# Optimization experiments

Hardware: AMD Instinct MI355X
Metric: run time of the kernel (lower is better)

Reference implementation:

```python
import jax, jax.numpy as jnp
import numpy as np

D = 1024
LD = 64
NTR = 8192
NT = 8192
DY = 128

def setup_inputs() -> dict:
    key = jax.random.key(0)
    k1, k2, k3, k4 = jax.random.split(key, 4)
    xtr = jax.random.normal(k1, (NTR, D), dtype=jnp.float32)
    ytr = jax.random.normal(k2, (NTR, DY), dtype=jnp.float32)
    xt = jax.random.normal(k3, (NT, D), dtype=jnp.float32)
    A = jax.random.normal(k4, (D, LD), dtype=jnp.float32) / (D ** 0.5)
    return {"xtr": xtr, "ytr": ytr, "xt": xt, "A": A}

def reference(xtr, ytr, xt, A):
    # mean-center both train and test features with the train mean
    mu = jnp.mean(xtr, axis=0, keepdims=True)          # [1, d]
    qtr = (xtr - mu) @ A                                # [Ntr, ld]
    qt = (xt - mu) @ A                                  # [Nt, ld]
    scores = jnp.einsum('nl,ml->nm', qt, qtr)           # [Nt, Ntr]
    E = jax.nn.softmax(scores, axis=1)                  # row-wise softmax over train points
    return E @ ytr                                      # [Nt, dy]
```

## Files before the change

kernel.cpp:

```cpp
#include <hip/hip_runtime.h>
#include <hip/hip_bf16.h>

#define D    1024
#define LD   64
#define NTR  8192
#define NT   8192
#define DY   128

#define SHIFT 40.0f

typedef __attribute__((ext_vector_type(8))) short bf16x8;
typedef __attribute__((ext_vector_type(8))) _Float16 half8;
typedef __attribute__((ext_vector_type(4))) short short4_;
typedef __attribute__((ext_vector_type(4))) float f4;

static __device__ __forceinline__ short f2bf(float f) {
    __hip_bfloat16 h = __float2bfloat16(f);
    short s; __builtin_memcpy(&s, &h, 2); return s;
}
static __device__ __forceinline__ float bf2f(short s) {
    __hip_bfloat16 h; __builtin_memcpy(&h, &s, 2); return __bfloat162float(h);
}
static __device__ __forceinline__ short f2h(float f) {
    _Float16 h = (_Float16)f;
    short s; __builtin_memcpy(&s, &h, 2); return s;
}
static __device__ __forceinline__ float h2f(short s) {
    _Float16 h; __builtin_memcpy(&h, &s, 2); return (float)h;
}

static __device__ __forceinline__ void gload_lds16(const void* g, void* l) {
    __builtin_amdgcn_global_load_lds(
        (const __attribute__((address_space(1))) unsigned int*)g,
        (__attribute__((address_space(3))) unsigned int*)l,
        16, 0, 0);
}

__global__ __launch_bounds__(256) void a_prep(const float* __restrict__ A,
                                              short* __restrict__ Afh,
                                              short* __restrict__ Afl) {
    int idx = blockIdx.x * 256 + threadIdx.x;
    float a = A[idx];
    int k = idx >> 6;
    int col = idx & 63;
    short hi = f2bf(a);
    short lo = f2bf(a - bf2f(hi));
    int o = ((k >> 6) * 8 + ((k >> 5) & 1) * 4 + ((k >> 3) & 3)) * 512
          + col * 8 + (k & 7);
    Afh[o] = hi;
    Afl[o] = lo;
}

__global__ __launch_bounds__(256) void proj_prep(const float* __restrict__ xt,
                                                 const float* __restrict__ xtr,
                                                 const short* __restrict__ Afh,
                                                 const short* __restrict__ Afl,
                                                 const float* __restrict__ ytr,
                                                 short* __restrict__ qt_hi,
                                                 short* __restrict__ qt_lo,
                                                 short* __restrict__ ktr,
                                                 float* __restrict__ muAp,
                                                 short* __restrict__ vtile) {
    __shared__ __align__(16) char smraw[32768];

    int tid = threadIdx.x;
    int b = blockIdx.x;

    if (b >= 512) {
        float* tile = (float*)smraw;
        int bz = b - 512;
        int t0 = (bz & 127) * 64;
        int d0 = (bz >> 7) * 64;
        int c = tid & 63;
        int r4 = tid >> 6;
        #pragma unroll
        for (int i = 0; i < 16; ++i) {
            int r = i * 4 + r4;
            tile[r * 66 + c] = ytr[(long)(t0 + r) * DY + d0 + c];
        }
        __syncthreads();
        #pragma unroll
        for (int i = 0; i < 16; ++i) {
            int r = i * 4 + r4;
            int t = t0 + c;
            int dy = d0 + r;
            long idx = (long)(t >> 5) * 4096 + (long)dy * 32
                     + ((((t >> 3) & 3) ^ (dy & 3)) << 3) + (t & 7);
            vtile[idx] = f2bf(tile[c * 66 + r]);
        }
        return;
    }

    short (*xh)[32][128] = (short (*)[32][128])smraw;
    short (*xl)[32][128] = (short (*)[32][128])(smraw + 16384);

    int wave = tid >> 6;
    int lane = tid & 63;
    int quad = lane >> 4;
    int l16 = lane & 15;

    bool is_test = b < 256;
    int row0 = (is_test ? b : b - 256) * 32;
    const float* x = is_test ? xt : xtr;

    int crow = tid >> 3;
    int cg0 = tid & 7;
    const float* xg = x + (long)(row0 + crow) * D + cg0 * 8;
    int sw0 = ((cg0)     ^ (crow & 7)) * 8;
    int sw1 = ((cg0 + 8) ^ (crow & 7)) * 8;

    int col = wave * 16 + l16;
    const short* AfhL = Afh + quad * 512 + col * 8;
    const short* AflL = Afl + quad * 512 + col * 8;

    f4 acc[2][2];
    #pragma unroll
    for (int rt = 0; rt < 2; ++rt)
        #pragma unroll
        for (int s2 = 0; s2 < 2; ++s2)
            acc[rt][s2] = (f4){0.f, 0.f, 0.f, 0.f};

    {
        f4 v0 = *(const f4*)xg;
        f4 v1 = *(const f4*)(xg + 4);
        f4 v2 = *(const f4*)(xg + 64);
        f4 v3 = *(const f4*)(xg + 68);
        bf16x8 h0, l0, h1, l1;
        #pragma unroll
        for (int e = 0; e < 4; ++e) {
            h0[e]     = f2bf(v0[e]);  l0[e]     = f2bf(v0[e] - bf2f(h0[e]));
            h0[e + 4] = f2bf(v1[e]);  l0[e + 4] = f2bf(v1[e] - bf2f(h0[e + 4]));
            h1[e]     = f2bf(v2[e]);  l1[e]     = f2bf(v2[e] - bf2f(h1[e]));
            h1[e + 4] = f2bf(v3[e]);  l1[e + 4] = f2bf(v3[e] - bf2f(h1[e + 4]));
        }
        *(bf16x8*)&xh[0][crow][sw0] = h0;
        *(bf16x8*)&xl[0][crow][sw0] = l0;
        *(bf16x8*)&xh[0][crow][sw1] = h1;
        *(bf16x8*)&xl[0][crow][sw1] = l1;
    }
    __syncthreads();

    #pragma unroll 1
    for (int s = 0; s < 8; ++s) {
        int cur = s & 1;

        f4 nv0, nv1, nv2, nv3;
        if (s < 7) {
            const float* ng = xg + (s + 1) * 128;
            nv0 = *(const f4*)ng;
            nv1 = *(const f4*)(ng + 4);
            nv2 = *(const f4*)(ng + 64);
            nv3 = *(const f4*)(ng + 68);
        }

        #pragma unroll
        for (int s2 = 0; s2 < 2; ++s2) {
            int s2g = s * 2 + s2;

            bf16x8 bh0 = *(const bf16x8*)(AfhL + s2g * 4096);
            bf16x8 bh1 = *(const bf16x8*)(AfhL + s2g * 4096 + 2048);
            bf16x8 bl0 = *(const bf16x8*)(AflL + s2g * 4096);
            bf16x8 bl1 = *(const bf16x8*)(AflL + s2g * 4096 + 2048);

            int ch0 = s2 * 8 + quad;
            int sx0 = ((ch0)     ^ (l16 & 7)) * 8;
            int sx1 = ((ch0 + 4) ^ (l16 & 7)) * 8;

            #pragma unroll
            for (int rt = 0; rt < 2; ++rt) {
                const short* xhr = &xh[cur][rt * 16 + l16][0];
                const short* xlr = &xl[cur][rt * 16 + l16][0];
                bf16x8 ah0 = *(const bf16x8*)(xhr + sx0);
                bf16x8 ah1 = *(const bf16x8*)(xhr + sx1);
                bf16x8 al0 = *(const bf16x8*)(xlr + sx0);
                bf16x8 al1 = *(const bf16x8*)(xlr + sx1);

                acc[rt][s2] = __builtin_amdgcn_mfma_f32_16x16x32_bf16(ah0, bh0, acc[rt][s2], 0, 0, 0);
                acc[rt][s2] = __builtin_amdgcn_mfma_f32_16x16x32_bf16(al0, bh0, acc[rt][s2], 0, 0, 0);
                acc[rt][s2] = __builtin_amdgcn_mfma_f32_16x16x32_bf16(ah0, bl0, acc[rt][s2], 0, 0, 0);
                acc[rt][s2] = __builtin_amdgcn_mfma_f32_16x16x32_bf16(ah1, bh1, acc[rt][s2], 0, 0, 0);
                acc[rt][s2] = __builtin_amdgcn_mfma_f32_16x16x32_bf16(al1, bh1, acc[rt][s2], 0, 0, 0);
                acc[rt][s2] = __builtin_amdgcn_mfma_f32_16x16x32_bf16(ah1, bl1, acc[rt][s2], 0, 0, 0);
            }
        }

        if (s < 7) {
            bf16x8 h0, l0, h1, l1;
            #pragma unroll
            for (int e = 0; e < 4; ++e) {
                h0[e]     = f2bf(nv0[e]);  l0[e]     = f2bf(nv0[e] - bf2f(h0[e]));
                h0[e + 4] = f2bf(nv1[e]);  l0[e + 4] = f2bf(nv1[e] - bf2f(h0[e + 4]));
                h1[e]     = f2bf(nv2[e]);  l1[e]     = f2bf(nv2[e] - bf2f(h1[e]));
                h1[e + 4] = f2bf(nv3[e]);  l1[e + 4] = f2bf(nv3[e] - bf2f(h1[e + 4]));
            }
            *(bf16x8*)&xh[cur ^ 1][crow][sw0] = h0;
            *(bf16x8*)&xl[cur ^ 1][crow][sw0] = l0;
            *(bf16x8*)&xh[cur ^ 1][crow][sw1] = h1;
            *(bf16x8*)&xl[cur ^ 1][crow][sw1] = l1;
        }
        __syncthreads();
    }

    #pragma unroll
    for (int rt = 0; rt < 2; ++rt) {
        f4 q4 = acc[rt][0] + acc[rt][1];
        #pragma unroll
        for (int r = 0; r < 4; ++r) {
            int grow = row0 + rt * 16 + quad * 4 + r;
            float qv = q4[r];
            if (is_test) {
                short hi = f2h(qv);
                qt_hi[(long)grow * LD + col] = hi;
                qt_lo[(long)grow * LD + col] = f2h(qv - h2f(hi));
            } else {
                int tl = grow & 31;
                long idx = (long)(grow >> 5) * 2048 + tl * 64
                         + ((((col >> 3) ^ (tl & 7))) << 3) + (col & 7);
                ktr[idx] = f2h(qv);
            }
        }
    }

    if (!is_test) {
        f4 t4 = (acc[0][0] + acc[0][1]) + (acc[1][0] + acc[1][1]);
        float s = t4[0] + t4[1] + t4[2] + t4[3];
        s += __shfl_xor(s, 16);
        s += __shfl_xor(s, 32);
        if (quad == 0) muAp[(long)(b - 256) * 64 + col] = s;
    }
}

__global__ __launch_bounds__(256) void c_kernel(const short* __restrict__ ktr,
                                                const float* __restrict__ muAp,
                                                float* __restrict__ cc) {
    __shared__ float red[4][64];
    __shared__ __align__(16) float muAs[64];
    int l = threadIdx.x & 63;
    int g = threadIdx.x >> 6;
    float ms = 0.f;
    #pragma unroll 8
    for (int p = g; p < 256; p += 4) ms += muAp[(long)p * 64 + l];
    red[g][l] = ms;
    __syncthreads();
    if (threadIdx.x < 64)
        muAs[l] = (red[0][l] + red[1][l] + red[2][l] + red[3][l]) *
                  (1.0f / (float)NTR);
    __syncthreads();

    int t = blockIdx.x * 256 + threadIdx.x;
    int tl = t & 31;
    long rb = (long)(t >> 5) * 2048 + tl * 64;
    float s = SHIFT;
    #pragma unroll
    for (int c = 0; c < 8; ++c) {
        int pos = (c ^ (tl & 7)) << 3;
        bf16x8 h8 = *(const bf16x8*)&ktr[rb + pos];
        f4 m0 = *(const f4*)&muAs[c * 8];
        f4 m1 = *(const f4*)&muAs[c * 8 + 4];
        #pragma unroll
        for (int j = 0; j < 4; ++j) {
            s += h2f(h8[j]) * m0[j];
            s += h2f(h8[j + 4]) * m1[j];
        }
    }
    cc[t] = s;
}

template<int NC>
__global__ __launch_bounds__(256, 3) void flash_kernel(const short* __restrict__ qt_hi,
                                                       const short* __restrict__ qt_lo,
                                                       const short* __restrict__ ksw,
                                                       const short* __restrict__ vtile,
                                                       const float* __restrict__ cc,
                                                       short* __restrict__ Opart,
                                                       float* __restrict__ Lpart) {
    constexpr int TPC = 256 / NC;
    constexpr int CH  = NTR / NC;

    __shared__ __align__(16) short kbh[2][2048];
    __shared__ __align__(16) short vbuf[2][4096];
    __shared__ __align__(16) short ptile[4][1280];

    int tid = threadIdx.x;
    int wave = tid >> 6;
    int lane = tid & 63;
    int quad = lane >> 4;
    int l16 = lane & 15;

    int kc = blockIdx.x & (NC - 1);
    int qi = blockIdx.x / NC;
    int q0w = qi * 128 + wave * 32;
    int tile0 = kc * TPC;
    int kc0 = kc * CH;

    int soff = wave * 512 + lane * 8;
    int ldso = wave * 512;

    half8 qh[2][2], ql[2][2];
    #pragma unroll
    for (int rt = 0; rt < 2; ++rt) {
        const short* qrh = qt_hi + (long)(q0w + rt * 16 + l16) * LD + quad * 8;
        const short* qrl = qt_lo + (long)(q0w + rt * 16 + l16) * LD + quad * 8;
        qh[rt][0] = *(const half8*)qrh;
        qh[rt][1] = *(const half8*)(qrh + 32);
        ql[rt][0] = *(const half8*)qrl;
        ql[rt][1] = *(const half8*)(qrl + 32);
    }

    bf16x8 onef;
    #pragma unroll
    for (int i = 0; i < 8; ++i) onef[i] = (short)0x3F80;

    f4 Ov[2][8];
    f4 Lv[2];
    #pragma unroll
    for (int rt = 0; rt < 2; ++rt) {
        Lv[rt] = (f4){0.f, 0.f, 0.f, 0.f};
        #pragma unroll
        for (int jt = 0; jt < 8; ++jt) Ov[rt][jt] = (f4){0.f, 0.f, 0.f, 0.f};
    }

    short* myp = &ptile[wave][0];
    const int p0 = ((quad ^ (l16 & 7)) << 3);
    const int pv = ((quad ^ (l16 & 3)) << 3);

    gload_lds16(ksw + (long)tile0 * 2048 + soff, &kbh[0][ldso]);
    gload_lds16(vtile + (long)tile0 * 4096 + soff, &vbuf[0][ldso]);
    gload_lds16(vtile + (long)tile0 * 4096 + 2048 + soff, &vbuf[0][2048 + ldso]);
    __syncthreads();

    #pragma unroll 1
    for (int it = 0; it < TPC; ++it) {
        int cur = it & 1;

        f4 cv[2];
        #pragma unroll
        for (int tt = 0; tt < 2; ++tt)
            cv[tt] = *(const f4*)&cc[kc0 + it * 32 + tt * 16 + quad * 4];

        if (it < TPC - 1) {
            int nb = cur ^ 1;
            long tb = (long)(tile0 + it + 1);
            gload_lds16(ksw + tb * 2048 + soff, &kbh[nb][ldso]);
            gload_lds16(vtile + tb * 4096 + soff, &vbuf[nb][ldso]);
            gload_lds16(vtile + tb * 4096 + 2048 + soff, &vbuf[nb][2048 + ldso]);
        }

        half8 kh[2][2];
        #pragma unroll
        for (int tt = 0; tt < 2; ++tt) {
            int rb = (tt * 16 + l16) * 64;
            kh[tt][0] = *(const half8*)&kbh[cur][rb + p0];
            kh[tt][1] = *(const half8*)&kbh[cur][rb + (p0 ^ 32)];
        }

        f4 s[2][2];
        #pragma unroll
        for (int rt = 0; rt < 2; ++rt) {
            #pragma unroll
            for (int tt = 0; tt < 2; ++tt) {
                f4 a = (f4){0.f, 0.f, 0.f, 0.f};
                a = __builtin_amdgcn_mfma_f32_16x16x32_f16(kh[tt][0], qh[rt][0], a, 0, 0, 0);
                a = __builtin_amdgcn_mfma_f32_16x16x32_f16(kh[tt][0], ql[rt][0], a, 0, 0, 0);
                a = __builtin_amdgcn_mfma_f32_16x16x32_f16(kh[tt][1], qh[rt][1], a, 0, 0, 0);
                a = __builtin_amdgcn_mfma_f32_16x16x32_f16(kh[tt][1], ql[rt][1], a, 0, 0, 0);
                s[rt][tt] = a;
            }
        }

        #pragma unroll
        for (int rt = 0; rt < 2; ++rt) {
            #pragma unroll
            for (int tt = 0; tt < 2; ++tt) {
                short4_ p4;
                p4[0] = f2bf(__expf(s[rt][tt][0] - cv[tt][0]));
                p4[1] = f2bf(__expf(s[rt][tt][1] - cv[tt][1]));
                p4[2] = f2bf(__expf(s[rt][tt][2] - cv[tt][2]));
                p4[3] = f2bf(__expf(s[rt][tt][3] - cv[tt][3]));
                *(short4_*)&myp[(rt * 16 + l16) * 40 + tt * 16 + quad * 4] = p4;
            }
        }

        bf16x8 vf[8];
        #pragma unroll
        for (int jt = 0; jt < 8; ++jt)
            vf[jt] = *(const bf16x8*)&vbuf[cur][(jt * 16 + l16) * 32 + pv];
        #pragma unroll
        for (int rt = 0; rt < 2; ++rt) {
            bf16x8 pf = *(const bf16x8*)&myp[(rt * 16 + l16) * 40 + quad * 8];
            #pragma unroll
            for (int jt = 0; jt < 8; ++jt)
                Ov[rt][jt] = __builtin_amdgcn_mfma_f32_16x16x32_bf16(pf, vf[jt], Ov[rt][jt], 0, 0, 0);
            Lv[rt] = __builtin_amdgcn_mfma_f32_16x16x32_bf16(pf, onef, Lv[rt], 0, 0, 0);
        }

        __syncthreads();
    }

    long ob = (long)kc * NT;
    #pragma unroll
    for (int rt = 0; rt < 2; ++rt) {
        #pragma unroll
        for (int jt = 0; jt < 8; ++jt) {
            #pragma unroll
            for (int r = 0; r < 4; ++r)
                Opart[(ob + q0w + rt * 16 + quad * 4 + r) * DY + jt * 16 + l16] =
                    f2bf(Ov[rt][jt][r]);
        }
        if (l16 == 0) {
            #pragma unroll
            for (int r = 0; r < 4; ++r)
                Lpart[ob + q0w + rt * 16 + quad * 4 + r] = Lv[rt][r];
        }
    }
}

template<int NC>
__global__ __launch_bounds__(256) void finalize_kernel(const short* __restrict__ Opart,
                                                       const float* __restrict__ Lpart,
                                                       float* __restrict__ out) {
    long i = ((long)blockIdx.x * 256 + threadIdx.x) * 8;
    long row = i >> 7;
    float L = 0.f;
    f4 a = (f4){0.f, 0.f, 0.f, 0.f};
    f4 b = (f4){0.f, 0.f, 0.f, 0.f};
    #pragma unroll
    for (int kc = 0; kc < NC; ++kc) {
        L += Lpart[(long)kc * NT + row];
        bf16x8 o = *(const bf16x8*)&Opart[(long)kc * NT * DY + i];
        #pragma unroll
        for (int j = 0; j < 4; ++j) {
            a[j] += bf2f(o[j]);
            b[j] += bf2f(o[j + 4]);
        }
    }
    float linv = 1.0f / L;
    a *= linv; b *= linv;
    *(f4*)&out[i] = a;
    *(f4*)&out[i + 4] = b;
}

extern "C" void kernel_launch(void* const* d_in, const int* in_sizes, int n_in,
                              void* d_out, int out_size, void* d_ws, size_t ws_size,
                              hipStream_t stream) {
    const float* xtr = (const float*)d_in[0];
    const float* ytr = (const float*)d_in[1];
    const float* xt  = (const float*)d_in[2];
    const float* A   = (const float*)d_in[3];
    float* out = (float*)d_out;

    const size_t need16 =
        (size_t)512 * 64 * 4 + (size_t)NTR * 4 +
        (size_t)16 * NT * 4 + (size_t)16 * NT * DY * 2 +
        (size_t)NT * LD * 2 * 2 + (size_t)NTR * LD * 2 +
        (size_t)DY * NTR * 2 + (size_t)D * LD * 2 * 2;
    const int NC = (ws_size >= need16) ? 16 : 8;

    char* w = (char*)d_ws;
    float* muAp  = (float*)w; w += (size_t)512 * 64 * 4;
    float* cc    = (float*)w; w += (size_t)NTR * 4;
    float* Lpart = (float*)w; w += (size_t)NC * NT * 4;
    short* Opart = (short*)w; w += (size_t)NC * NT * DY * 2;
    short* qt_hi  = (short*)w; w += (size_t)NT * LD * 2;
    short* qt_lo  = (short*)w; w += (size_t)NT * LD * 2;
    short* ksw    = (short*)w; w += (size_t)NTR * LD * 2;
    short* vtile  = (short*)w; w += (size_t)DY * NTR * 2;
    short* Afh    = (short*)w; w += (size_t)D * LD * 2;
    short* Afl    = (short*)w; w += (size_t)D * LD * 2;
    (void)in_sizes; (void)n_in; (void)out_size;

    a_prep<<<256, 256, 0, stream>>>(A, Afh, Afl);
    proj_prep<<<768, 256, 0, stream>>>(xt, xtr, Afh, Afl, ytr,
                                       qt_hi, qt_lo, ksw, muAp, vtile);
    c_kernel<<<32, 256, 0, stream>>>(ksw, muAp, cc);
    if (NC == 16) {
        flash_kernel<16><<<64 * 16, 256, 0, stream>>>(qt_hi, qt_lo, ksw, vtile,
                                                      cc, Opart, Lpart);
        finalize_kernel<16><<<(NT * DY) / (256 * 8), 256, 0, stream>>>(Opart,
                                                                       Lpart, out);
    } else {
        flash_kernel<8><<<64 * 8, 256, 0, stream>>>(qt_hi, qt_lo, ksw, vtile,
                                                    cc, Opart, Lpart);
        finalize_kernel<8><<<(NT * DY) / (256 * 8), 256, 0, stream>>>(Opart,
                                                                      Lpart, out);
    }
}
```

Before: 161.6 us.

## Merge prep and flash/finalize stages into cooperative kernels with grid sync

Replaces the five separate launches with two cooperative kernels: one runs A prep, projection and the c-shift computation separated by grid-wide syncs, the other runs the flash attention pass with NC=8 followed by a grid sync and the finalize reduction. The aim is to cut kernel launch gaps and tail idle time between stages. The flash path now always uses 8 key chunks, giving 512 blocks instead of 1024, which lowers parallelism. It also relies on every block being co-resident for the grid sync, and falls back to separate launches if the cooperative launch fails.

```diff
diff --git a/kernel.cpp b/kernel.cpp
--- a/kernel.cpp
+++ b/kernel.cpp
@@ -1,5 +1,8 @@
 #include <hip/hip_runtime.h>
 #include <hip/hip_bf16.h>
+#include <hip/hip_cooperative_groups.h>
+
+namespace cg = cooperative_groups;
 
 #define D    1024
 #define LD   64
@@ -36,10 +39,11 @@
         16, 0, 0);
 }
 
-__global__ __launch_bounds__(256) void a_prep(const float* __restrict__ A,
-                                              short* __restrict__ Afh,
-                                              short* __restrict__ Afl) {
-    int idx = blockIdx.x * 256 + threadIdx.x;
+
+static __device__ __forceinline__ void aprep_body(const float* __restrict__ A,
+                                                  short* __restrict__ Afh,
+                                                  short* __restrict__ Afl,
+                                                  int idx) {
     float a = A[idx];
     int k = idx >> 6;
     int col = idx & 63;
@@ -51,20 +55,18 @@
     Afl[o] = lo;
 }
 
-__global__ __launch_bounds__(256) void proj_prep(const float* __restrict__ xt,
-                                                 const float* __restrict__ xtr,
-                                                 const short* __restrict__ Afh,
-                                                 const short* __restrict__ Afl,
-                                                 const float* __restrict__ ytr,
-                                                 short* __restrict__ qt_hi,
-                                                 short* __restrict__ qt_lo,
-                                                 short* __restrict__ ktr,
-                                                 float* __restrict__ muAp,
-                                                 short* __restrict__ vtile) {
+static __device__ void proj_body(const float* __restrict__ xt,
+                                 const float* __restrict__ xtr,
+                                 const short* __restrict__ Afh,
+                                 const short* __restrict__ Afl,
+                                 const float* __restrict__ ytr,
+                                 short* __restrict__ qt_hi,
+                                 short* __restrict__ qt_lo,
+                                 short* __restrict__ ktr,
+                                 float* __restrict__ muAp,
+                                 short* __restrict__ vtile,
+                                 int b, int tid) {
     __shared__ __align__(16) char smraw[32768];
-
-    int tid = threadIdx.x;
-    int b = blockIdx.x;
 
     if (b >= 512) {
         float* tile = (float*)smraw;
@@ -230,24 +232,24 @@
     }
 }
 
-__global__ __launch_bounds__(256) void c_kernel(const short* __restrict__ ktr,
-                                                const float* __restrict__ muAp,
-                                                float* __restrict__ cc) {
+static __device__ void c_body(const short* __restrict__ ktr,
+                              const float* __restrict__ muAp,
+                              float* __restrict__ cc, int bid, int tid) {
     __shared__ float red[4][64];
     __shared__ __align__(16) float muAs[64];
-    int l = threadIdx.x & 63;
-    int g = threadIdx.x >> 6;
+    int l = tid & 63;
+    int g = tid >> 6;
     float ms = 0.f;
     #pragma unroll 8
     for (int p = g; p < 256; p += 4) ms += muAp[(long)p * 64 + l];
     red[g][l] = ms;
     __syncthreads();
-    if (threadIdx.x < 64)
+    if (tid < 64)
         muAs[l] = (red[0][l] + red[1][l] + red[2][l] + red[3][l]) *
                   (1.0f / (float)NTR);
     __syncthreads();
 
-    int t = blockIdx.x * 256 + threadIdx.x;
+    int t = bid * 256 + tid;
     int tl = t & 31;
     long rb = (long)(t >> 5) * 2048 + tl * 64;
     float s = SHIFT;
@@ -264,6 +266,242 @@
         }
     }
     cc[t] = s;
+}
+
+template<int NC>
+static __device__ void flash_body(const short* __restrict__ qt_hi,
+                                  const short* __restrict__ qt_lo,
+                                  const short* __restrict__ ksw,
+                                  const short* __restrict__ vtile,
+                                  const float* __restrict__ cc,
+                                  short* __restrict__ Opart,
+                                  float* __restrict__ Lpart,
+                                  int bid, int tid) {
+    constexpr int TPC = 256 / NC;
+    constexpr int CH  = NTR / NC;
+
+    __shared__ __align__(16) short kbh[2][2048];
+    __shared__ __align__(16) short vbuf[2][4096];
+    __shared__ __align__(16) short ptile[4][1280];
+
+    int wave = tid >> 6;
+    int lane = tid & 63;
+    int quad = lane >> 4;
+    int l16 = lane & 15;
+
+    int kc = bid & (NC - 1);
+    int qi = bid / NC;
+    int q0w = qi * 128 + wave * 32;
+    int tile0 = kc * TPC;
+    int kc0 = kc * CH;
+
+    int soff = wave * 512 + lane * 8;
+    int ldso = wave * 512;
+
+    half8 qh[2][2], ql[2][2];
+    #pragma unroll
+    for (int rt = 0; rt < 2; ++rt) {
+        const short* qrh = qt_hi + (long)(q0w + rt * 16 + l16) * LD + quad * 8;
+        const short* qrl = qt_lo + (long)(q0w + rt * 16 + l16) * LD + quad * 8;
+        qh[rt][0] = *(const half8*)qrh;
+        qh[rt][1] = *(const half8*)(qrh + 32);
+        ql[rt][0] = *(const half8*)qrl;
+        ql[rt][1] = *(const half8*)(qrl + 32);
+    }
+
+    bf16x8 onef;
+    #pragma unroll
+    for (int i = 0; i < 8; ++i) onef[i] = (short)0x3F80;
+
+    f4 Ov[2][8];
+    f4 Lv[2];
+    #pragma unroll
+    for (int rt = 0; rt < 2; ++rt) {
+        Lv[rt] = (f4){0.f, 0.f, 0.f, 0.f};
+        #pragma unroll
+        for (int jt = 0; jt < 8; ++jt) Ov[rt][jt] = (f4){0.f, 0.f, 0.f, 0.f};
+    }
+
+    short* myp = &ptile[wave][0];
+    const int p0 = ((quad ^ (l16 & 7)) << 3);
+    const int pv = ((quad ^ (l16 & 3)) << 3);
+
+    gload_lds16(ksw + (long)tile0 * 2048 + soff, &kbh[0][ldso]);
+    gload_lds16(vtile + (long)tile0 * 4096 + soff, &vbuf[0][ldso]);
+    gload_lds16(vtile + (long)tile0 * 4096 + 2048 + soff, &vbuf[0][2048 + ldso]);
+    __syncthreads();
+
+    #pragma unroll 1
+    for (int it = 0; it < TPC; ++it) {
+        int cur = it & 1;
+
+        f4 cv[2];
+        #pragma unroll
+        for (int tt = 0; tt < 2; ++tt)
+            cv[tt] = *(const f4*)&cc[kc0 + it * 32 + tt * 16 + quad * 4];
+
+        if (it < TPC - 1) {
+            int nb = cur ^ 1;
+            long tb = (long)(tile0 + it + 1);
+            gload_lds16(ksw + tb * 2048 + soff, &kbh[nb][ldso]);
+            gload_lds16(vtile + tb * 4096 + soff, &vbuf[nb][ldso]);
+            gload_lds16(vtile + tb * 4096 + 2048 + soff, &vbuf[nb][2048 + ldso]);
+        }
+
+        half8 kh[2][2];
+        #pragma unroll
+        for (int tt = 0; tt < 2; ++tt) {
+            int rb = (tt * 16 + l16) * 64;
+            kh[tt][0] = *(const half8*)&kbh[cur][rb + p0];
+            kh[tt][1] = *(const half8*)&kbh[cur][rb + (p0 ^ 32)];
+        }
+
+        f4 s[2][2];
+        #pragma unroll
+        for (int rt = 0; rt < 2; ++rt) {
+            #pragma unroll
+            for (int tt = 0; tt < 2; ++tt) {
+                f4 a = (f4){0.f, 0.f, 0.f, 0.f};
+                a = __builtin_amdgcn_mfma_f32_16x16x32_f16(kh[tt][0], qh[rt][0], a, 0, 0, 0);
+                a = __builtin_amdgcn_mfma_f32_16x16x32_f16(kh[tt][0], ql[rt][0], a, 0, 0, 0);
+                a = __builtin_amdgcn_mfma_f32_16x16x32_f16(kh[tt][1], qh[rt][1], a, 0, 0, 0);
+                a = __builtin_amdgcn_mfma_f32_16x16x32_f16(kh[tt][1], ql[rt][1], a, 0, 0, 0);
+                s[rt][tt] = a;
+            }
+        }
+
+        #pragma unroll
+        for (int rt = 0; rt < 2; ++rt) {
+            #pragma unroll
+            for (int tt = 0; tt < 2; ++tt) {
+                short4_ p4;
+                p4[0] = f2bf(__expf(s[rt][tt][0] - cv[tt][0]));
+                p4[1] = f2bf(__expf(s[rt][tt][1] - cv[tt][1]));
+                p4[2] = f2bf(__expf(s[rt][tt][2] - cv[tt][2]));
+                p4[3] = f2bf(__expf(s[rt][tt][3] - cv[tt][3]));
+                *(short4_*)&myp[(rt * 16 + l16) * 40 + tt * 16 + quad * 4] = p4;
+            }
+        }
+
+        bf16x8 vf[8];
+        #pragma unroll
+        for (int jt = 0; jt < 8; ++jt)
+            vf[jt] = *(const bf16x8*)&vbuf[cur][(jt * 16 + l16) * 32 + pv];
+        #pragma unroll
+        for (int rt = 0; rt < 2; ++rt) {
+            bf16x8 pf = *(const bf16x8*)&myp[(rt * 16 + l16) * 40 + quad * 8];
+            #pragma unroll
+            for (int jt = 0; jt < 8; ++jt)
+                Ov[rt][jt] = __builtin_amdgcn_mfma_f32_16x16x32_bf16(pf, vf[jt], Ov[rt][jt], 0, 0, 0);
+            Lv[rt] = __builtin_amdgcn_mfma_f32_16x16x32_bf16(pf, onef, Lv[rt], 0, 0, 0);
+        }
+
+        __syncthreads();
+    }
+
+    long ob = (long)kc * NT;
+    #pragma unroll
+    for (int rt = 0; rt < 2; ++rt) {
+        #pragma unroll
+        for (int jt = 0; jt < 8; ++jt) {
+            #pragma unroll
+            for (int r = 0; r < 4; ++r)
+                Opart[(ob + q0w + rt * 16 + quad * 4 + r) * DY + jt * 16 + l16] =
+                    f2bf(Ov[rt][jt][r]);
+        }
+        if (l16 == 0) {
+            #pragma unroll
+            for (int r = 0; r < 4; ++r)
+                Lpart[ob + q0w + rt * 16 + quad * 4 + r] = Lv[rt][r];
+        }
+    }
+}
+
+template<int NC>
+static __device__ void finalize_body(const short* __restrict__ Opart,
+                                     const float* __restrict__ Lpart,
+                                     float* __restrict__ out, int bid, int tid) {
+    long i = ((long)bid * 256 + tid) * 8;
+    long row = i >> 7;
+    float L = 0.f;
+    f4 a = (f4){0.f, 0.f, 0.f, 0.f};
+    f4 b = (f4){0.f, 0.f, 0.f, 0.f};
+    #pragma unroll
+    for (int kc = 0; kc < NC; ++kc) {
+        L += Lpart[(long)kc * NT + row];
+        bf16x8 o = *(const bf16x8*)&Opart[(long)kc * NT * DY + i];
+        #pragma unroll
+        for (int j = 0; j < 4; ++j) {
+            a[j] += bf2f(o[j]);
+            b[j] += bf2f(o[j + 4]);
+        }
+    }
+    float linv = 1.0f / L;
+    a *= linv; b *= linv;
+    *(f4*)&out[i] = a;
+    *(f4*)&out[i + 4] = b;
+}
+
+
+__global__ __launch_bounds__(256, 3) void prep_all(const float* __restrict__ xt,
+                                                   const float* __restrict__ xtr,
+                                                   const float* __restrict__ A,
+                                                   const float* __restrict__ ytr,
+                                                   short* __restrict__ qt_hi,
+                                                   short* __restrict__ qt_lo,
+                                                   short* __restrict__ ktr,
+                                                   float* __restrict__ muAp,
+                                                   short* __restrict__ vtile,
+                                                   short* __restrict__ Afh,
+                                                   short* __restrict__ Afl,
+                                                   float* __restrict__ cc) {
+    int gi = blockIdx.x * 256 + threadIdx.x;
+    if (gi < 65536) aprep_body(A, Afh, Afl, gi);
+    cg::this_grid().sync();
+    proj_body(xt, xtr, Afh, Afl, ytr, qt_hi, qt_lo, ktr, muAp, vtile,
+              blockIdx.x, threadIdx.x);
+    cg::this_grid().sync();
+    if (blockIdx.x < 32) c_body(ktr, muAp, cc, blockIdx.x, threadIdx.x);
+}
+
+__global__ __launch_bounds__(256, 3) void flash_fin(const short* __restrict__ qt_hi,
+                                                    const short* __restrict__ qt_lo,
+                                                    const short* __restrict__ ksw,
+                                                    const short* __restrict__ vtile,
+                                                    const float* __restrict__ cc,
+                                                    short* __restrict__ Opart,
+                                                    float* __restrict__ Lpart,
+                                                    float* __restrict__ out) {
+    flash_body<8>(qt_hi, qt_lo, ksw, vtile, cc, Opart, Lpart,
+                  blockIdx.x, threadIdx.x);
+    cg::this_grid().sync();
+    finalize_body<8>(Opart, Lpart, out, blockIdx.x, threadIdx.x);
+}
+
+__global__ __launch_bounds__(256) void a_prep(const float* __restrict__ A,
+                                              short* __restrict__ Afh,
+                                              short* __restrict__ Afl) {
+    aprep_body(A, Afh, Afl, blockIdx.x * 256 + threadIdx.x);
+}
+
+__global__ __launch_bounds__(256) void proj_prep(const float* __restrict__ xt,
+                                                 const float* __restrict__ xtr,
+                                                 const short* __restrict__ Afh,
+                                                 const short* __restrict__ Afl,
+                                                 const float* __restrict__ ytr,
+                                                 short* __restrict__ qt_hi,
+                                                 short* __restrict__ qt_lo,
+                                                 short* __restrict__ ktr,
+                                                 float* __restrict__ muAp,
+                                                 short* __restrict__ vtile) {
+    proj_body(xt, xtr, Afh, Afl, ytr, qt_hi, qt_lo, ktr, muAp, vtile,
+              blockIdx.x, threadIdx.x);
+}
+
+__global__ __launch_bounds__(256) void c_kernel(const short* __restrict__ ktr,
+                                                const float* __restrict__ muAp,
+                                                float* __restrict__ cc) {
+    c_body(ktr, muAp, cc, blockIdx.x, threadIdx.x);
 }
 
 template<int NC>
@@ -274,170 +512,15 @@
                                                        const float* __restrict__ cc,
                                                        short* __restrict__ Opart,
                                                        float* __restrict__ Lpart) {
-    constexpr int TPC = 256 / NC;
-    constexpr int CH  = NTR / NC;
-
-    __shared__ __align__(16) short kbh[2][2048];
-    __shared__ __align__(16) short vbuf[2][4096];
-    __shared__ __align__(16) short ptile[4][1280];
-
-    int tid = threadIdx.x;
-    int wave = tid >> 6;
-    int lane = tid & 63;
-    int quad = lane >> 4;
-    int l16 = lane & 15;
-
-    int kc = blockIdx.x & (NC - 1);
-    int qi = blockIdx.x / NC;
-    int q0w = qi * 128 + wave * 32;
-    int tile0 = kc * TPC;
-    int kc0 = kc * CH;
-
-    int soff = wave * 512 + lane * 8;
-    int ldso = wave * 512;
-
-    half8 qh[2][2], ql[2][2];
-    #pragma unroll
-    for (int rt = 0; rt < 2; ++rt) {
-        const short* qrh = qt_hi + (long)(q0w + rt * 16 + l16) * LD + quad * 8;
-        const short* qrl = qt_lo + (long)(q0w + rt * 16 + l16) * LD + quad * 8;
-        qh[rt][0] = *(const half8*)qrh;
-        qh[rt][1] = *(const half8*)(qrh + 32);
-        ql[rt][0] = *(const half8*)qrl;
-        ql[rt][1] = *(const half8*)(qrl + 32);
-    }
-
-    bf16x8 onef;
-    #pragma unroll
-    for (int i = 0; i < 8; ++i) onef[i] = (short)0x3F80;
-
-    f4 Ov[2][8];
-    f4 Lv[2];
-    #pragma unroll
-    for (int rt = 0; rt < 2; ++rt) {
-        Lv[rt] = (f4){0.f, 0.f, 0.f, 0.f};
-        #pragma unroll
-        for (int jt = 0; jt < 8; ++jt) Ov[rt][jt] = (f4){0.f, 0.f, 0.f, 0.f};
-    }
-
-    short* myp = &ptile[wave][0];
-    const int p0 = ((quad ^ (l16 & 7)) << 3);
-    const int pv = ((quad ^ (l16 & 3)) << 3);
-
-    gload_lds16(ksw + (long)tile0 * 2048 + soff, &kbh[0][ldso]);
-    gload_lds16(vtile + (long)tile0 * 4096 + soff, &vbuf[0][ldso]);
-    gload_lds16(vtile + (long)tile0 * 4096 + 2048 + soff, &vbuf[0][2048 + ldso]);
-    __syncthreads();
-
-    #pragma unroll 1
-    for (int it = 0; it < TPC; ++it) {
-        int cur = it & 1;
-
-        f4 cv[2];
-        #pragma unroll
-        for (int tt = 0; tt < 2; ++tt)
-            cv[tt] = *(const f4*)&cc[kc0 + it * 32 + tt * 16 + quad * 4];
-
-        if (it < TPC - 1) {
-            int nb = cur ^ 1;
-            long tb = (long)(tile0 + it + 1);
-            gload_lds16(ksw + tb * 2048 + soff, &kbh[nb][ldso]);
-            gload_lds16(vtile + tb * 4096 + soff, &vbuf[nb][ldso]);
-            gload_lds16(vtile + tb * 4096 + 2048 + soff, &vbuf[nb][2048 + ldso]);
-        }
-
-        half8 kh[2][2];
-        #pragma unroll
-        for (int tt = 0; tt < 2; ++tt) {
-            int rb = (tt * 16 + l16) * 64;
-            kh[tt][0] = *(const half8*)&kbh[cur][rb + p0];
-            kh[tt][1] = *(const half8*)&kbh[cur][rb + (p0 ^ 32)];
-        }
-
-        f4 s[2][2];
-        #pragma unroll
-        for (int rt = 0; rt < 2; ++rt) {
-            #pragma unroll
-            for (int tt = 0; tt < 2; ++tt) {
-                f4 a = (f4){0.f, 0.f, 0.f, 0.f};
-                a = __builtin_amdgcn_mfma_f32_16x16x32_f16(kh[tt][0], qh[rt][0], a, 0, 0, 0);
-                a = __builtin_amdgcn_mfma_f32_16x16x32_f16(kh[tt][0], ql[rt][0], a, 0, 0, 0);
-                a = __builtin_amdgcn_mfma_f32_16x16x32_f16(kh[tt][1], qh[rt][1], a, 0, 0, 0);
-                a = __builtin_amdgcn_mfma_f32_16x16x32_f16(kh[tt][1], ql[rt][1], a, 0, 0, 0);
-                s[rt][tt] = a;
-            }
-        }
-
-        #pragma unroll
-        for (int rt = 0; rt < 2; ++rt) {
-            #pragma unroll
-            for (int tt = 0; tt < 2; ++tt) {
-                short4_ p4;
-                p4[0] = f2bf(__expf(s[rt][tt][0] - cv[tt][0]));
-                p4[1] = f2bf(__expf(s[rt][tt][1] - cv[tt][1]));
-                p4[2] = f2bf(__expf(s[rt][tt][2] - cv[tt][2]));
-                p4[3] = f2bf(__expf(s[rt][tt][3] - cv[tt][3]));
-                *(short4_*)&myp[(rt * 16 + l16) * 40 + tt * 16 + quad * 4] = p4;
-            }
-        }
-
-        bf16x8 vf[8];
-        #pragma unroll
-        for (int jt = 0; jt < 8; ++jt)
-            vf[jt] = *(const bf16x8*)&vbuf[cur][(jt * 16 + l16) * 32 + pv];
-        #pragma unroll
-        for (int rt = 0; rt < 2; ++rt) {
-            bf16x8 pf = *(const bf16x8*)&myp[(rt * 16 + l16) * 40 + quad * 8];
-            #pragma unroll
-            for (int jt = 0; jt < 8; ++jt)
-                Ov[rt][jt] = __builtin_amdgcn_mfma_f32_16x16x32_bf16(pf, vf[jt], Ov[rt][jt], 0, 0, 0);
-            Lv[rt] = __builtin_amdgcn_mfma_f32_16x16x32_bf16(pf, onef, Lv[rt], 0, 0, 0);
-        }
-
-        __syncthreads();
-    }
-
-    long ob = (long)kc * NT;
-    #pragma unroll
-    for (int rt = 0; rt < 2; ++rt) {
-        #pragma unroll
-        for (int jt = 0; jt < 8; ++jt) {
-            #pragma unroll
-            for (int r = 0; r < 4; ++r)
-                Opart[(ob + q0w + rt * 16 + quad * 4 + r) * DY + jt * 16 + l16] =
-                    f2bf(Ov[rt][jt][r]);
-        }
-        if (l16 == 0) {
-            #pragma unroll
-            for (int r = 0; r < 4; ++r)
-                Lpart[ob + q0w + rt * 16 + quad * 4 + r] = Lv[rt][r];
-        }
-    }
+    flash_body<NC>(qt_hi, qt_lo, ksw, vtile, cc, Opart, Lpart,
+                   blockIdx.x, threadIdx.x);
 }
 
 template<int NC>
 __global__ __launch_bounds__(256) void finalize_kernel(const short* __restrict__ Opart,
                                                        const float* __restrict__ Lpart,
                                                        float* __restrict__ out) {
-    long i = ((long)blockIdx.x * 256 + threadIdx.x) * 8;
-    long row = i >> 7;
-    float L = 0.f;
-    f4 a = (f4){0.f, 0.f, 0.f, 0.f};
-    f4 b = (f4){0.f, 0.f, 0.f, 0.f};
-    #pragma unroll
-    for (int kc = 0; kc < NC; ++kc) {
-        L += Lpart[(long)kc * NT + row];
-        bf16x8 o = *(const bf16x8*)&Opart[(long)kc * NT * DY + i];
-        #pragma unroll
-        for (int j = 0; j < 4; ++j) {
-            a[j] += bf2f(o[j]);
-            b[j] += bf2f(o[j + 4]);
-        }
-    }
-    float linv = 1.0f / L;
-    a *= linv; b *= linv;
-    *(f4*)&out[i] = a;
-    *(f4*)&out[i + 4] = b;
+    finalize_body<NC>(Opart, Lpart, out, blockIdx.x, threadIdx.x);
 }
 
 extern "C" void kernel_launch(void* const* d_in, const int* in_sizes, int n_in,
@@ -454,13 +537,13 @@
         (size_t)16 * NT * 4 + (size_t)16 * NT * DY * 2 +
         (size_t)NT * LD * 2 * 2 + (size_t)NTR * LD * 2 +
         (size_t)DY * NTR * 2 + (size_t)D * LD * 2 * 2;
-    const int NC = (ws_size >= need16) ? 16 : 8;
+    const int NCF = (ws_size >= need16) ? 16 : 8;
 
     char* w = (char*)d_ws;
     float* muAp  = (float*)w; w += (size_t)512 * 64 * 4;
     float* cc    = (float*)w; w += (size_t)NTR * 4;
-    float* Lpart = (float*)w; w += (size_t)NC * NT * 4;
-    short* Opart = (short*)w; w += (size_t)NC * NT * DY * 2;
+    float* Lpart = (float*)w; w += (size_t)NCF * NT * 4;
+    short* Opart = (short*)w; w += (size_t)NCF * NT * DY * 2;
     short* qt_hi  = (short*)w; w += (size_t)NT * LD * 2;
     short* qt_lo  = (short*)w; w += (size_t)NT * LD * 2;
     short* ksw    = (short*)w; w += (size_t)NTR * LD * 2;
@@ -469,19 +552,41 @@
     short* Afl    = (short*)w; w += (size_t)D * LD * 2;
     (void)in_sizes; (void)n_in; (void)out_size;
 
-    a_prep<<<256, 256, 0, stream>>>(A, Afh, Afl);
-    proj_prep<<<768, 256, 0, stream>>>(xt, xtr, Afh, Afl, ytr,
-                                       qt_hi, qt_lo, ksw, muAp, vtile);
-    c_kernel<<<32, 256, 0, stream>>>(ksw, muAp, cc);
-    if (NC == 16) {
-        flash_kernel<16><<<64 * 16, 256, 0, stream>>>(qt_hi, qt_lo, ksw, vtile,
-                                                      cc, Opart, Lpart);
-        finalize_kernel<16><<<(NT * DY) / (256 * 8), 256, 0, stream>>>(Opart,
-                                                                       Lpart, out);
-    } else {
-        flash_kernel<8><<<64 * 8, 256, 0, stream>>>(qt_hi, qt_lo, ksw, vtile,
-                                                    cc, Opart, Lpart);
-        finalize_kernel<8><<<(NT * DY) / (256 * 8), 256, 0, stream>>>(Opart,
-                                                                      Lpart, out);
-    }
-}
+    {
+        void* a1[] = {(void*)&xt, (void*)&xtr, (void*)&A, (void*)&ytr,
+                      (void*)&qt_hi, (void*)&qt_lo, (void*)&ksw, (void*)&muAp,
+                      (void*)&vtile, (void*)&Afh, (void*)&Afl, (void*)&cc};
+        hipError_t e = hipLaunchCooperativeKernel((const void*)prep_all,
+                                                  dim3(768), dim3(256),
+                                                  a1, 0, stream);
+        if (e != hipSuccess) {
+            a_prep<<<256, 256, 0, stream>>>(A, Afh, Afl);
+            proj_prep<<<768, 256, 0, stream>>>(xt, xtr, Afh, Afl, ytr,
+                                               qt_hi, qt_lo, ksw, muAp, vtile);
+            c_kernel<<<32, 256, 0, stream>>>(ksw, muAp, cc);
+        }
+    }
+
+    {
+        void* a2[] = {(void*)&qt_hi, (void*)&qt_lo, (void*)&ksw, (void*)&vtile,
+                      (void*)&cc, (void*)&Opart, (void*)&Lpart, (void*)&out};
+        hipError_t e = hipLaunchCooperativeKernel((const void*)flash_fin,
+                                                  dim3(512), dim3(256),
+                                                  a2, 0, stream);
+        if (e != hipSuccess) {
+            if (NCF == 16) {
+                flash_kernel<16><<<64 * 16, 256, 0, stream>>>(qt_hi, qt_lo, ksw,
+                                                              vtile, cc, Opart,
+                                                              Lpart);
+                finalize_kernel<16><<<(NT * DY) / (256 * 8), 256, 0, stream>>>(
+                    Opart, Lpart, out);
+            } else {
+                flash_kernel<8><<<64 * 8, 256, 0, stream>>>(qt_hi, qt_lo, ksw,
+                                                            vtile, cc, Opart,
+                                                            Lpart);
+                finalize_kernel<8><<<(NT * DY) / (256 * 8), 256, 0, stream>>>(
+                    Opart, Lpart, out);
+            }
+        }
+    }
+}
```

Result: slower. 431.5 us (+167.0%).

## Fuse A-split prep into projection and per-key bias into flash kernel

Applied to the files above, without the earlier changes.

Removes the a_prep and c_kernel launches. The projection kernel now reads fp32 A directly with strided scalar loads and splits it into bf16 hi/lo in registers, and each flash block recomputes the mean reduction and its chunk of per-key bias terms into shared memory. This saves two kernel launches and workspace traffic. In exchange it adds redundant work: every projection block re-splits A with uncoalesced loads, and each of the 1024 flash blocks re-reduces muAp and adds extra LDS.

```diff
diff --git a/kernel.cpp b/kernel.cpp
--- a/kernel.cpp
+++ b/kernel.cpp
@@ -36,25 +36,9 @@
         16, 0, 0);
 }
 
-__global__ __launch_bounds__(256) void a_prep(const float* __restrict__ A,
-                                              short* __restrict__ Afh,
-                                              short* __restrict__ Afl) {
-    int idx = blockIdx.x * 256 + threadIdx.x;
-    float a = A[idx];
-    int k = idx >> 6;
-    int col = idx & 63;
-    short hi = f2bf(a);
-    short lo = f2bf(a - bf2f(hi));
-    int o = ((k >> 6) * 8 + ((k >> 5) & 1) * 4 + ((k >> 3) & 3)) * 512
-          + col * 8 + (k & 7);
-    Afh[o] = hi;
-    Afl[o] = lo;
-}
-
 __global__ __launch_bounds__(256) void proj_prep(const float* __restrict__ xt,
                                                  const float* __restrict__ xtr,
-                                                 const short* __restrict__ Afh,
-                                                 const short* __restrict__ Afl,
+                                                 const float* __restrict__ A,
                                                  const float* __restrict__ ytr,
                                                  short* __restrict__ qt_hi,
                                                  short* __restrict__ qt_lo,
@@ -110,8 +94,7 @@
     int sw1 = ((cg0 + 8) ^ (crow & 7)) * 8;
 
     int col = wave * 16 + l16;
-    const short* AfhL = Afh + quad * 512 + col * 8;
-    const short* AflL = Afl + quad * 512 + col * 8;
+    const float* Acol = A + col;
 
     f4 acc[2][2];
     #pragma unroll
@@ -156,11 +139,18 @@
         #pragma unroll
         for (int s2 = 0; s2 < 2; ++s2) {
             int s2g = s * 2 + s2;
-
-            bf16x8 bh0 = *(const bf16x8*)(AfhL + s2g * 4096);
-            bf16x8 bh1 = *(const bf16x8*)(AfhL + s2g * 4096 + 2048);
-            bf16x8 bl0 = *(const bf16x8*)(AflL + s2g * 4096);
-            bf16x8 bl1 = *(const bf16x8*)(AflL + s2g * 4096 + 2048);
+            int k0 = s2g * 64;
+
+            bf16x8 bh0, bh1, bl0, bl1;
+            #pragma unroll
+            for (int j = 0; j < 8; ++j) {
+                float a0 = Acol[(k0 + quad * 8 + j) * LD];
+                float a1 = Acol[(k0 + 32 + quad * 8 + j) * LD];
+                short hh0 = f2bf(a0);
+                short hh1 = f2bf(a1);
+                bh0[j] = hh0; bl0[j] = f2bf(a0 - bf2f(hh0));
+                bh1[j] = hh1; bl1[j] = f2bf(a1 - bf2f(hh1));
+            }
 
             int ch0 = s2 * 8 + quad;
             int sx0 = ((ch0)     ^ (l16 & 7)) * 8;
@@ -230,48 +220,12 @@
     }
 }
 
-__global__ __launch_bounds__(256) void c_kernel(const short* __restrict__ ktr,
-                                                const float* __restrict__ muAp,
-                                                float* __restrict__ cc) {
-    __shared__ float red[4][64];
-    __shared__ __align__(16) float muAs[64];
-    int l = threadIdx.x & 63;
-    int g = threadIdx.x >> 6;
-    float ms = 0.f;
-    #pragma unroll 8
-    for (int p = g; p < 256; p += 4) ms += muAp[(long)p * 64 + l];
-    red[g][l] = ms;
-    __syncthreads();
-    if (threadIdx.x < 64)
-        muAs[l] = (red[0][l] + red[1][l] + red[2][l] + red[3][l]) *
-                  (1.0f / (float)NTR);
-    __syncthreads();
-
-    int t = blockIdx.x * 256 + threadIdx.x;
-    int tl = t & 31;
-    long rb = (long)(t >> 5) * 2048 + tl * 64;
-    float s = SHIFT;
-    #pragma unroll
-    for (int c = 0; c < 8; ++c) {
-        int pos = (c ^ (tl & 7)) << 3;
-        bf16x8 h8 = *(const bf16x8*)&ktr[rb + pos];
-        f4 m0 = *(const f4*)&muAs[c * 8];
-        f4 m1 = *(const f4*)&muAs[c * 8 + 4];
-        #pragma unroll
-        for (int j = 0; j < 4; ++j) {
-            s += h2f(h8[j]) * m0[j];
-            s += h2f(h8[j + 4]) * m1[j];
-        }
-    }
-    cc[t] = s;
-}
-
 template<int NC>
 __global__ __launch_bounds__(256, 3) void flash_kernel(const short* __restrict__ qt_hi,
                                                        const short* __restrict__ qt_lo,
                                                        const short* __restrict__ ksw,
                                                        const short* __restrict__ vtile,
-                                                       const float* __restrict__ cc,
+                                                       const float* __restrict__ muAp,
                                                        short* __restrict__ Opart,
                                                        float* __restrict__ Lpart) {
     constexpr int TPC = 256 / NC;
@@ -280,6 +234,9 @@
     __shared__ __align__(16) short kbh[2][2048];
     __shared__ __align__(16) short vbuf[2][4096];
     __shared__ __align__(16) short ptile[4][1280];
+    __shared__ __align__(16) float ccs[CH];
+    __shared__ float redm[4][64];
+    __shared__ __align__(16) float muAs[64];
 
     int tid = threadIdx.x;
     int wave = tid >> 6;
@@ -292,6 +249,42 @@
     int q0w = qi * 128 + wave * 32;
     int tile0 = kc * TPC;
     int kc0 = kc * CH;
+
+    {
+        int l = tid & 63;
+        int g = tid >> 6;
+        float ms = 0.f;
+        #pragma unroll 8
+        for (int p = g; p < 256; p += 4) ms += muAp[(long)p * 64 + l];
+        redm[g][l] = ms;
+        __syncthreads();
+        if (tid < 64)
+            muAs[l] = (redm[0][l] + redm[1][l] + redm[2][l] + redm[3][l]) *
+                      (1.0f / (float)NTR);
+        __syncthreads();
+
+        #pragma unroll
+        for (int u = 0; u < CH / 256; ++u) {
+            int t = kc0 + u * 256 + tid;
+            int tl = t & 31;
+            long rb = (long)(t >> 5) * 2048 + tl * 64;
+            float s = SHIFT;
+            #pragma unroll
+            for (int c = 0; c < 8; ++c) {
+                int pos = (c ^ (tl & 7)) << 3;
+                bf16x8 h8 = *(const bf16x8*)&ksw[rb + pos];
+                f4 m0 = *(const f4*)&muAs[c * 8];
+                f4 m1 = *(const f4*)&muAs[c * 8 + 4];
+                #pragma unroll
+                for (int j = 0; j < 4; ++j) {
+                    s += h2f(h8[j]) * m0[j];
+                    s += h2f(h8[j + 4]) * m1[j];
+                }
+            }
+            ccs[u * 256 + tid] = s;
+        }
+        __syncthreads();
+    }
 
     int soff = wave * 512 + lane * 8;
     int ldso = wave * 512;
@@ -336,7 +329,7 @@
         f4 cv[2];
         #pragma unroll
         for (int tt = 0; tt < 2; ++tt)
-            cv[tt] = *(const f4*)&cc[kc0 + it * 32 + tt * 16 + quad * 4];
+            cv[tt] = *(const f4*)&ccs[it * 32 + tt * 16 + quad * 4];
 
         if (it < TPC - 1) {
             int nb = cur ^ 1;
@@ -450,37 +443,32 @@
     float* out = (float*)d_out;
 
     const size_t need16 =
-        (size_t)512 * 64 * 4 + (size_t)NTR * 4 +
+        (size_t)512 * 64 * 4 +
         (size_t)16 * NT * 4 + (size_t)16 * NT * DY * 2 +
         (size_t)NT * LD * 2 * 2 + (size_t)NTR * LD * 2 +
-        (size_t)DY * NTR * 2 + (size_t)D * LD * 2 * 2;
+        (size_t)DY * NTR * 2;
     const int NC = (ws_size >= need16) ? 16 : 8;
 
     char* w = (char*)d_ws;
     float* muAp  = (float*)w; w += (size_t)512 * 64 * 4;
-    float* cc    = (float*)w; w += (size_t)NTR * 4;
     float* Lpart = (float*)w; w += (size_t)NC * NT * 4;
     short* Opart = (short*)w; w += (size_t)NC * NT * DY * 2;
     short* qt_hi  = (short*)w; w += (size_t)NT * LD * 2;
     short* qt_lo  = (short*)w; w += (size_t)NT * LD * 2;
     short* ksw    = (short*)w; w += (size_t)NTR * LD * 2;
     short* vtile  = (short*)w; w += (size_t)DY * NTR * 2;
-    short* Afh    = (short*)w; w += (size_t)D * LD * 2;
-    short* Afl    = (short*)w; w += (size_t)D * LD * 2;
     (void)in_sizes; (void)n_in; (void)out_size;
 
-    a_prep<<<256, 256, 0, stream>>>(A, Afh, Afl);
-    proj_prep<<<768, 256, 0, stream>>>(xt, xtr, Afh, Afl, ytr,
+    proj_prep<<<768, 256, 0, stream>>>(xt, xtr, A, ytr,
                                        qt_hi, qt_lo, ksw, muAp, vtile);
-    c_kernel<<<32, 256, 0, stream>>>(ksw, muAp, cc);
     if (NC == 16) {
         flash_kernel<16><<<64 * 16, 256, 0, stream>>>(qt_hi, qt_lo, ksw, vtile,
-                                                      cc, Opart, Lpart);
+                                                      muAp, Opart, Lpart);
         finalize_kernel<16><<<(NT * DY) / (256 * 8), 256, 0, stream>>>(Opart,
                                                                        Lpart, out);
     } else {
         flash_kernel<8><<<64 * 8, 256, 0, stream>>>(qt_hi, qt_lo, ksw, vtile,
-                                                    cc, Opart, Lpart);
+                                                    muAp, Opart, Lpart);
         finalize_kernel<8><<<(NT * DY) / (256 * 8), 256, 0, stream>>>(Opart,
                                                                       Lpart, out);
     }
```

Measured after the change: 187.5 us. +16.0%, slower.

## Fuse split-K finalize into flash kernel via last-block atomic counter

Applied to the files above, without the earlier changes.

Removes the separate finalize kernel launch. Each flash block bumps a per-query-tile atomic counter after writing its partial O and L, and the last block to finish for that tile reduces all NC partials and writes the normalized output. This saves a launch and overlaps the reduction with the tail of the flash kernel. In exchange it adds threadfences, an atomic per block, a memset of the counters, and a serialized reduction in the last-arriving block.

```diff
diff --git a/kernel.cpp b/kernel.cpp
--- a/kernel.cpp
+++ b/kernel.cpp
@@ -273,13 +273,16 @@
                                                        const short* __restrict__ vtile,
                                                        const float* __restrict__ cc,
                                                        short* __restrict__ Opart,
-                                                       float* __restrict__ Lpart) {
+                                                       float* __restrict__ Lpart,
+                                                       int* __restrict__ done,
+                                                       float* __restrict__ out) {
     constexpr int TPC = 256 / NC;
     constexpr int CH  = NTR / NC;
 
     __shared__ __align__(16) short kbh[2][2048];
     __shared__ __align__(16) short vbuf[2][4096];
     __shared__ __align__(16) short ptile[4][1280];
+    __shared__ int lastflag;
 
     int tid = threadIdx.x;
     int wave = tid >> 6;
@@ -413,31 +416,38 @@
                 Lpart[ob + q0w + rt * 16 + quad * 4 + r] = Lv[rt][r];
         }
     }
-}
-
-template<int NC>
-__global__ __launch_bounds__(256) void finalize_kernel(const short* __restrict__ Opart,
-                                                       const float* __restrict__ Lpart,
-                                                       float* __restrict__ out) {
-    long i = ((long)blockIdx.x * 256 + threadIdx.x) * 8;
-    long row = i >> 7;
-    float L = 0.f;
-    f4 a = (f4){0.f, 0.f, 0.f, 0.f};
-    f4 b = (f4){0.f, 0.f, 0.f, 0.f};
-    #pragma unroll
-    for (int kc = 0; kc < NC; ++kc) {
-        L += Lpart[(long)kc * NT + row];
-        bf16x8 o = *(const bf16x8*)&Opart[(long)kc * NT * DY + i];
-        #pragma unroll
-        for (int j = 0; j < 4; ++j) {
-            a[j] += bf2f(o[j]);
-            b[j] += bf2f(o[j + 4]);
-        }
-    }
-    float linv = 1.0f / L;
-    a *= linv; b *= linv;
-    *(f4*)&out[i] = a;
-    *(f4*)&out[i + 4] = b;
+
+    __threadfence();
+    __syncthreads();
+    if (tid == 0)
+        lastflag = (atomicAdd(&done[qi], 1) == NC - 1);
+    __syncthreads();
+    if (lastflag) {
+        __threadfence();
+        #pragma unroll 1
+        for (int u = 0; u < 8; ++u) {
+            int idx = u * 256 + tid;
+            long row = (long)qi * 128 + (idx >> 4);
+            long i = row * DY + (idx & 15) * 8;
+            float L = 0.f;
+            f4 a = (f4){0.f, 0.f, 0.f, 0.f};
+            f4 b2 = (f4){0.f, 0.f, 0.f, 0.f};
+            #pragma unroll
+            for (int k2 = 0; k2 < NC; ++k2) {
+                L += Lpart[(long)k2 * NT + row];
+                bf16x8 o = *(const bf16x8*)&Opart[(long)k2 * NT * DY + i];
+                #pragma unroll
+                for (int j = 0; j < 4; ++j) {
+                    a[j]  += bf2f(o[j]);
+                    b2[j] += bf2f(o[j + 4]);
+                }
+            }
+            float linv = 1.0f / L;
+            a *= linv; b2 *= linv;
+            *(f4*)&out[i] = a;
+            *(f4*)&out[i + 4] = b2;
+        }
+    }
 }
 
 extern "C" void kernel_launch(void* const* d_in, const int* in_sizes, int n_in,
@@ -450,13 +460,14 @@
     float* out = (float*)d_out;
 
     const size_t need16 =
-        (size_t)512 * 64 * 4 + (size_t)NTR * 4 +
+        512 + (size_t)512 * 64 * 4 + (size_t)NTR * 4 +
         (size_t)16 * NT * 4 + (size_t)16 * NT * DY * 2 +
         (size_t)NT * LD * 2 * 2 + (size_t)NTR * LD * 2 +
         (size_t)DY * NTR * 2 + (size_t)D * LD * 2 * 2;
     const int NC = (ws_size >= need16) ? 16 : 8;
 
     char* w = (char*)d_ws;
+    int*   done  = (int*)w;   w += 512;
     float* muAp  = (float*)w; w += (size_t)512 * 64 * 4;
     float* cc    = (float*)w; w += (size_t)NTR * 4;
     float* Lpart = (float*)w; w += (size_t)NC * NT * 4;
@@ -469,19 +480,16 @@
     short* Afl    = (short*)w; w += (size_t)D * LD * 2;
     (void)in_sizes; (void)n_in; (void)out_size;
 
+    hipMemsetAsync(done, 0, 64 * sizeof(int), stream);
     a_prep<<<256, 256, 0, stream>>>(A, Afh, Afl);
     proj_prep<<<768, 256, 0, stream>>>(xt, xtr, Afh, Afl, ytr,
                                        qt_hi, qt_lo, ksw, muAp, vtile);
     c_kernel<<<32, 256, 0, stream>>>(ksw, muAp, cc);
     if (NC == 16) {
         flash_kernel<16><<<64 * 16, 256, 0, stream>>>(qt_hi, qt_lo, ksw, vtile,
-                                                      cc, Opart, Lpart);
-        finalize_kernel<16><<<(NT * DY) / (256 * 8), 256, 0, stream>>>(Opart,
-                                                                       Lpart, out);
+                                                      cc, Opart, Lpart, done, out);
     } else {
         flash_kernel<8><<<64 * 8, 256, 0, stream>>>(qt_hi, qt_lo, ksw, vtile,
-                                                    cc, Opart, Lpart);
-        finalize_kernel<8><<<(NT * DY) / (256 * 8), 256, 0, stream>>>(Opart,
-                                                                      Lpart, out);
-    }
-}
+                                                    cc, Opart, Lpart, done, out);
+    }
+}
```

Result: slower. 396.9 us (+145.6%).
